# Kernel optimization log

Measured on AMD Instinct MI355X. Metric: run time of the kernel, lower is better.

## Reference

```python
import jax, jax.numpy as jnp
import numpy as np

B, EMB, HID, IN_DIM, STEP = 4096, 256, 256, 128, 128


def setup_inputs() -> dict:
    key = jax.random.key(0)
    ks = jax.random.split(key, 9)
    s1 = 1.0 / np.sqrt(HID)   # torch LSTMCell init: U(-1/sqrt(hidden), 1/sqrt(hidden))
    s2 = 1.0 / np.sqrt(IN_DIM)
    u = lambda k, shape, s: jax.random.uniform(k, shape, jnp.float32, -s, s)
    return {
        "emb_inp": jax.random.normal(ks[0], (B, EMB), jnp.float32),
        # cell1: LSTMCell(EMB -> HID), gate order i,f,g,o
        "W_ih1": u(ks[1], (4 * HID, EMB), s1),
        "W_hh1": u(ks[2], (4 * HID, HID), s1),
        "b_ih1": u(ks[3], (4 * HID,), s1),
        "b_hh1": u(ks[4], (4 * HID,), s1),
        # cell2: LSTMCell(HID -> IN_DIM)
        "W_ih2": u(ks[5], (4 * IN_DIM, HID), s2),
        "W_hh2": u(ks[6], (4 * IN_DIM, IN_DIM), s2),
        "b_ih2": u(ks[7], (4 * IN_DIM,), s2),
        "b_hh2": u(ks[8], (4 * IN_DIM,), s2),
    }


def _lstm_gates(gates, c):
    # torch.nn.LSTMCell gate order: input, forget, cell(g), output
    i, f, g, o = jnp.split(gates, 4, axis=-1)
    c_new = jax.nn.sigmoid(f) * c + jax.nn.sigmoid(i) * jnp.tanh(g)
    h_new = jax.nn.sigmoid(o) * jnp.tanh(c_new)
    return h_new, c_new


def reference(emb_inp, W_ih1, W_hh1, b_ih1, b_hh1, W_ih2, W_hh2, b_ih2, b_hh2):
    batch = emb_inp.shape[0]
    hid = W_hh1.shape[1]
    in_dim = W_hh2.shape[1]
    dt = emb_inp.dtype
    # the same emb_inp is fed at every step -> precompute input-gate preactivations once
    x1 = emb_inp @ W_ih1.T + b_ih1 + b_hh1              # [B, 4*HID]
    b2 = b_ih2 + b_hh2

    init = (jnp.zeros((batch, hid), dt), jnp.zeros((batch, hid), dt),
            jnp.zeros((batch, in_dim), dt), jnp.zeros((batch, in_dim), dt))

    def step_fn(carry, _):
        h0, c0, h1, c1 = carry
        h0, c0 = _lstm_gates(x1 + h0 @ W_hh1.T, c0)
        h1, c1 = _lstm_gates(h0 @ W_ih2.T + b2 + h1 @ W_hh2.T, c1)
        return (h0, c0, h1, c1), h1

    _, ys = jax.lax.scan(step_fn, init, None, length=STEP)  # [STEP, B, IN_DIM]
    return jnp.transpose(ys, (1, 0, 2))                     # [B, STEP, IN_DIM]
```

## Files before the change

kernel.cpp:

```cpp
#include <hip/hip_runtime.h>

typedef __attribute__((ext_vector_type(8))) short bf16x8;
typedef __attribute__((ext_vector_type(4))) short bf16x4;
typedef __attribute__((ext_vector_type(4))) float f32x4;

__device__ __forceinline__ short f2bf(float f) {
  union { float f; unsigned u; } v; v.f = f;
  unsigned r = v.u + 0x7fffu + ((v.u >> 16) & 1u);
  return (short)(r >> 16);
}
__device__ __forceinline__ float sigm(float x) {
  float e = exp2f(-1.44269504f * x);
  return __builtin_amdgcn_rcpf(1.0f + e);
}
__device__ __forceinline__ float tanh_f(float x) {
  float e = exp2f(-2.88539008f * x);
  return __builtin_fmaf(2.0f, __builtin_amdgcn_rcpf(1.0f + e), -1.0f);
}
__device__ __forceinline__ f32x4 splat4(float b){ f32x4 v = {b,b,b,b}; return v; }

__device__ __forceinline__ void ld_b128_sc0(bf16x8* d, const void* p) {
  asm volatile("global_load_dwordx4 %0, %1, off sc0" : "=&v"(*d) : "v"(p));
}
__device__ __forceinline__ void vm_drain_sched() {
  asm volatile("s_waitcnt vmcnt(0)" ::: "memory");
  __builtin_amdgcn_sched_barrier(0);
}

#define R1S   0
#define R2AS  262144
#define R2BS  393216
#define R1IS  458752
#define CTRL_B 1441792
#define H0X_B  1462272
#define H1X_B  5656576

#define H0S 57344
#define H1S 65536
#define OUTS 69632

__global__ __launch_bounds__(256) void pack_w(
    const float* __restrict__ W_ih1, const float* __restrict__ W_hh1,
    const float* __restrict__ W_ih2, const float* __restrict__ W_hh2,
    short* __restrict__ wp) {
  int s = blockIdx.x * 256 + threadIdx.x;
  if (blockIdx.x == 0) {
    unsigned* c = (unsigned*)((char*)wp + CTRL_B);
    #pragma unroll
    for (int k = 0; k < 20; ++k) c[threadIdx.x + k * 256] = 0u;
  }
  if (s >= 90112) return;
  const float* src; int row, K, k0, l;
  if (s < 32768) {
    int mm = s >> 11, r = s & 2047, g = r >> 9, kc = (r >> 6) & 7; l = r & 63;
    row = g*256 + mm*16 + (l & 15); K = 256; k0 = kc*32 + (l>>4)*8; src = W_hh1;
  } else if (s < 49152) {
    int s2 = s - 32768, mm = s2 >> 10, r = s2 & 1023, gh = r >> 9, kc = (r >> 6) & 7; l = r & 63;
    int ul = (l & 15) >> 1, gp = l & 1;
    row = (gh*2+gp)*128 + mm*8 + ul; K = 256; k0 = kc*32 + (l>>4)*8; src = W_ih2;
  } else if (s < 57344) {
    int s3 = s - 49152, mm = s3 >> 9, r = s3 & 511, gh = r >> 8, kc = (r >> 6) & 3; l = r & 63;
    int ul = (l & 15) >> 1, gp = l & 1;
    row = (gh*2+gp)*128 + mm*8 + ul; K = 128; k0 = kc*32 + (l>>4)*8; src = W_hh2;
  } else {
    int s4 = s - 57344, mm = s4 >> 11, r = s4 & 2047, g = r >> 9, kc = (r >> 6) & 7; l = r & 63;
    row = g*256 + mm*16 + (l & 15); K = 256; k0 = kc*32 + (l>>4)*8; src = W_ih1;
  }
  const float* p = src + (size_t)row * K + k0;
  bf16x8 o;
  #pragma unroll
  for (int e = 0; e < 8; ++e) o[e] = f2bf(p[e]);
  *(bf16x8*)(wp + (size_t)s * 8) = o;
}

__global__ __launch_bounds__(512, 2) void lstm_persist(
    const float* __restrict__ emb, const float* __restrict__ b_ih1,
    const float* __restrict__ b_hh1, const float* __restrict__ b_ih2,
    const float* __restrict__ b_hh2, char* __restrict__ ws,
    float* __restrict__ out) {
  extern __shared__ __align__(16) short ldsW[];
  char* ldsB = (char*)ldsW;
  const short* wp = (const short*)ws;
  unsigned* ctrl = (unsigned*)(ws + CTRL_B);
  __shared__ unsigned s_gm;
  const int tid = threadIdx.x, w = tid >> 6, l = tid & 63, l15 = l & 15, l4 = l >> 4;
  const int ul = l15 >> 1, gp = l15 & 1;

  if (tid == 0) {
    unsigned xcc;
    asm volatile("s_getreg_b32 %0, hwreg(HW_REG_XCC_ID)" : "=s"(xcc));
    xcc &= 7u;
    unsigned slot = atomicAdd(&ctrl[xcc * 32], 1u);
    s_gm = ((xcc * 2u + ((slot >> 4) & 1u)) << 8) | (slot & 15u);
  }
  __syncthreads();
  const int group = s_gm >> 8, member = s_gm & 255;

  {
    const char* wpB = (const char*)wp;
    #pragma unroll
    for (int it = 0; it < 7; ++it) {
      int byte = (tid + it * 512) * 16;
      const char* src;
      if (byte < 32768)      src = wpB + (size_t)R1S * 2  + member * 32768 + byte;
      else if (byte < 49152) src = wpB + (size_t)R2AS * 2 + member * 16384 + (byte - 32768);
      else                   src = wpB + (size_t)R2BS * 2 + member * 8192  + (byte - 49152);
      *(f32x4*)(ldsB + byte) = *(const f32x4*)src;
    }
  }
  float b2[2];
  #pragma unroll
  for (int gh = 0; gh < 2; ++gh) {
    int rw = (gh*2+gp)*128 + member*8 + ul;
    b2[gh] = b_ih2[rw] + b_hh2[rw];
  }
  float b1[4];
  #pragma unroll
  for (int g = 0; g < 4; ++g) {
    int rw = g*256 + member*16 + l15;
    b1[g] = b_ih1[rw] + b_hh1[rw];
  }
  __syncthreads();

  const int grow0 = group * 256;
  const int rw0 = w * 32;
  f32x4 x1[2][4];
  #pragma unroll
  for (int m = 0; m < 2; ++m)
    #pragma unroll
    for (int g = 0; g < 4; ++g) x1[m][g] = splat4(b1[g]);
  #pragma unroll
  for (int kc = 0; kc < 8; ++kc) {
    bf16x8 af[2];
    #pragma unroll
    for (int m = 0; m < 2; ++m) {
      const float* ep = emb + (size_t)(grow0 + rw0 + m*16 + l15) * 256 + kc*32 + l4*8;
      f32x4 lo = *(const f32x4*)ep, hi = *(const f32x4*)(ep + 4);
      bf16x8 t8;
      #pragma unroll
      for (int e = 0; e < 4; ++e) { t8[e] = f2bf(lo[e]); t8[e+4] = f2bf(hi[e]); }
      af[m] = t8;
    }
    #pragma unroll
    for (int g = 0; g < 4; ++g) {
      bf16x8 bb = *(const bf16x8*)(wp + R1IS + (((size_t)member*4 + g)*8 + kc)*512 + l*8);
      x1[0][g] = __builtin_amdgcn_mfma_f32_16x16x32_bf16(af[0], bb, x1[0][g], 0, 0, 0);
      x1[1][g] = __builtin_amdgcn_mfma_f32_16x16x32_bf16(af[1], bb, x1[1][g], 0, 0, 0);
    }
  }

  bf16x8 a0[2][8], a1[2][4];
  const bf16x8 ZB = {0,0,0,0,0,0,0,0};
  #pragma unroll
  for (int m = 0; m < 2; ++m) {
    #pragma unroll
    for (int kc = 0; kc < 8; ++kc) a0[m][kc] = ZB;
    #pragma unroll
    for (int kc = 0; kc < 4; ++kc) a1[m][kc] = ZB;
  }
  float c0[2][4] = {};
  float c1[2][2] = {};

  unsigned* flgA = &ctrl[512 + group * 64];
  unsigned* flgB = flgA + 32;
  char* h0x = ws + H0X_B;
  char* h1x = ws + H1X_B;

  #pragma unroll 1
  for (int u = 0; u <= 128; ++u) {
    if (u < 128) {
      vm_drain_sched();
      f32x4 acc1[2][4];
      #pragma unroll
      for (int m = 0; m < 2; ++m)
        #pragma unroll
        for (int g = 0; g < 4; ++g) acc1[m][g] = x1[m][g];
      #pragma unroll
      for (int g = 0; g < 4; ++g)
        #pragma unroll
        for (int kc = 0; kc < 8; ++kc) {
          bf16x8 bb = *(const bf16x8*)(ldsW + (g*8 + kc)*512 + l*8);
          acc1[0][g] = __builtin_amdgcn_mfma_f32_16x16x32_bf16(a0[0][kc], bb, acc1[0][g], 0,0,0);
          acc1[1][g] = __builtin_amdgcn_mfma_f32_16x16x32_bf16(a0[1][kc], bb, acc1[1][g], 0,0,0);
        }
      #pragma unroll
      for (int m = 0; m < 2; ++m)
        #pragma unroll
        for (int r = 0; r < 4; ++r) {
          float iv = acc1[m][0][r], fv = acc1[m][1][r];
          float gv = acc1[m][2][r], ov = acc1[m][3][r];
          float c = sigm(fv) * c0[m][r] + sigm(iv) * tanh_f(gv);
          c0[m][r] = c;
          float h = sigm(ov) * tanh_f(c);
          int row = rw0 + m*16 + l4*4 + r;
          *(short*)(ldsB + H0S + row*32 + l15*2) = f2bf(h);
        }
      {
        char* h0w = h0x + ((size_t)(u & 1) * 16 + group) * 131072;
        int prow = rw0 + (l >> 1);
        int off = prow*32 + (l & 1)*16;
        bf16x8 v = *(const bf16x8*)(ldsB + H0S + off);
        *(bf16x8*)(h0w + member*8192 + off) = v;
      }
      asm volatile("s_waitcnt vmcnt(0)" ::: "memory");
      __syncthreads();
      if (tid == 0)
        __hip_atomic_store(&flgA[member], (unsigned)(u + 1),
                           __ATOMIC_RELAXED, __HIP_MEMORY_SCOPE_AGENT);
    }
    f32x4 acc2[2][2];
    if (u >= 1) {
      if (u >= 2) {
        unsigned tgt = (unsigned)(u - 1); int z = 0;
        while (true) {
          unsigned v = __hip_atomic_load(&flgB[l15], __ATOMIC_RELAXED, __HIP_MEMORY_SCOPE_AGENT);
          if (__all((int)(v >= tgt))) break;
          __builtin_amdgcn_s_sleep(1);
          if (++z > (1 << 20)) break;
        }
        __builtin_amdgcn_sched_barrier(0);
        const char* h1r = h1x + ((size_t)((u - 2) & 1) * 16 + group) * 65536;
        #pragma unroll
        for (int m = 0; m < 2; ++m)
          #pragma unroll
          for (int kc = 0; kc < 4; ++kc)
            ld_b128_sc0(&a1[m][kc], h1r + (kc*4 + l4)*4096 + (rw0 + m*16 + l15)*16);
        vm_drain_sched();
      }
      #pragma unroll
      for (int m = 0; m < 2; ++m)
        #pragma unroll
        for (int gh = 0; gh < 2; ++gh) acc2[m][gh] = splat4(b2[gh]);
      #pragma unroll
      for (int gh = 0; gh < 2; ++gh)
        #pragma unroll
        for (int kc = 0; kc < 8; ++kc) {
          bf16x8 bb = *(const bf16x8*)(ldsW + 16384 + (gh*8 + kc)*512 + l*8);
          acc2[0][gh] = __builtin_amdgcn_mfma_f32_16x16x32_bf16(a0[0][kc], bb, acc2[0][gh], 0,0,0);
          acc2[1][gh] = __builtin_amdgcn_mfma_f32_16x16x32_bf16(a0[1][kc], bb, acc2[1][gh], 0,0,0);
        }
      #pragma unroll
      for (int gh = 0; gh < 2; ++gh)
        #pragma unroll
        for (int kc = 0; kc < 4; ++kc) {
          bf16x8 bb = *(const bf16x8*)(ldsW + 24576 + (gh*4 + kc)*512 + l*8);
          acc2[0][gh] = __builtin_amdgcn_mfma_f32_16x16x32_bf16(a1[0][kc], bb, acc2[0][gh], 0,0,0);
          acc2[1][gh] = __builtin_amdgcn_mfma_f32_16x16x32_bf16(a1[1][kc], bb, acc2[1][gh], 0,0,0);
        }
    }
    if (u < 128) {
      unsigned tgt = (unsigned)(u + 1); int z = 0;
      while (true) {
        unsigned v = __hip_atomic_load(&flgA[l15], __ATOMIC_RELAXED, __HIP_MEMORY_SCOPE_AGENT);
        if (__all((int)(v >= tgt))) break;
        __builtin_amdgcn_s_sleep(1);
        if (++z > (1 << 20)) break;
      }
      __builtin_amdgcn_sched_barrier(0);
      const char* h0r = h0x + ((size_t)(u & 1) * 16 + group) * 131072;
      #pragma unroll
      for (int m = 0; m < 2; ++m)
        #pragma unroll
        for (int kc = 0; kc < 8; ++kc)
          ld_b128_sc0(&a0[m][kc],
                      h0r + (kc*2 + (l4 >> 1))*8192 + (rw0 + m*16 + l15)*32 + (l4 & 1)*16);
      __builtin_amdgcn_sched_barrier(0);
    }
    if (u >= 1) {
      const int t = u - 1;
      #pragma unroll
      for (int m = 0; m < 2; ++m) {
        f32x4 v0 = acc2[m][0], v1 = acc2[m][1];
        #pragma unroll
        for (int rr = 0; rr < 2; ++rr) {
          float s0 = gp ? v0[rr] : v0[2+rr];
          float s1 = gp ? v1[rr] : v1[2+rr];
          float p0 = __shfl_xor(s0, 1, 64);
          float p1 = __shfl_xor(s1, 1, 64);
          float o0 = gp ? v0[2+rr] : v0[rr];
          float o1 = gp ? v1[2+rr] : v1[rr];
          float iv = gp ? p0 : o0, fv = gp ? o0 : p0;
          float gv = gp ? p1 : o1, ov = gp ? o1 : p1;
          float c = sigm(fv) * c1[m][rr] + sigm(iv) * tanh_f(gv);
          c1[m][rr] = c;
          float h = sigm(ov) * tanh_f(c);
          int row = rw0 + m*16 + l4*4 + gp*2 + rr;
          *(short*)(ldsB + H1S + row*16 + ul*2) = f2bf(h);
          *(float*)(ldsB + OUTS + row*32 + ul*4) = h;
        }
      }
      if (u < 128) {
        char* h1w = h1x + ((size_t)(t & 1) * 16 + group) * 65536;
        int prow = rw0 + (l >> 1);
        int off = prow*16 + (l & 1)*8;
        bf16x4 v = *(const bf16x4*)(ldsB + H1S + off);
        *(bf16x4*)(h1w + member*4096 + off) = v;
        asm volatile("s_waitcnt vmcnt(0)" ::: "memory");
        __syncthreads();
        if (tid == 0)
          __hip_atomic_store(&flgB[member], (unsigned)u,
                             __ATOMIC_RELAXED, __HIP_MEMORY_SCOPE_AGENT);
      }
      {
        int prow = rw0 + (l >> 1);
        f32x4 v = *(const f32x4*)(ldsB + OUTS + prow*32 + (l & 1)*16);
        float* op = out + (size_t)(grow0 + prow) * 16384 + t*128 + member*8 + (l & 1)*4;
        __builtin_nontemporal_store(v, (f32x4*)op);
      }
    }
  }
}

extern "C" void kernel_launch(void* const* d_in, const int* in_sizes, int n_in,
                              void* d_out, int out_size, void* d_ws, size_t ws_size,
                              hipStream_t stream) {
  const float* emb   = (const float*)d_in[0];
  const float* W_ih1 = (const float*)d_in[1];
  const float* W_hh1 = (const float*)d_in[2];
  const float* b_ih1 = (const float*)d_in[3];
  const float* b_hh1 = (const float*)d_in[4];
  const float* W_ih2 = (const float*)d_in[5];
  const float* W_hh2 = (const float*)d_in[6];
  const float* b_ih2 = (const float*)d_in[7];
  const float* b_hh2 = (const float*)d_in[8];
  char* ws = (char*)d_ws;
  float* out = (float*)d_out;

  hipFuncSetAttribute((const void*)lstm_persist,
                      hipFuncAttributeMaxDynamicSharedMemorySize, 98304);
  pack_w<<<352, 256, 0, stream>>>(W_ih1, W_hh1, W_ih2, W_hh2, (short*)d_ws);
  lstm_persist<<<256, 512, 98304, stream>>>(emb, b_ih1, b_hh1, b_ih2, b_hh2, ws, out);
}
```

Baseline: 881.6 us.

## Merge two per-step cross-workgroup barriers into one combined flag sync

Replaces the separate flgA/flgB flag handshakes for h0 and h1 with a single per-step flag. Each step now computes cell1 and cell2, publishes both hidden states, and signals once. It then waits once and loads both the next h0 and h1 operands together. This halves the number of global spin-wait barriers on the recurrent critical path, but removes the overlap between the cell2 MMA and the h0 exchange wait.

```diff
diff --git a/kernel.cpp b/kernel.cpp
--- a/kernel.cpp
+++ b/kernel.cpp
@@ -161,15 +161,13 @@
   float c0[2][4] = {};
   float c1[2][2] = {};
 
-  unsigned* flgA = &ctrl[512 + group * 64];
-  unsigned* flgB = flgA + 32;
+  unsigned* flg = &ctrl[512 + group * 64];
   char* h0x = ws + H0X_B;
   char* h1x = ws + H1X_B;
 
   #pragma unroll 1
   for (int u = 0; u <= 128; ++u) {
     if (u < 128) {
-      vm_drain_sched();
       f32x4 acc1[2][4];
       #pragma unroll
       for (int m = 0; m < 2; ++m)
@@ -202,31 +200,10 @@
         bf16x8 v = *(const bf16x8*)(ldsB + H0S + off);
         *(bf16x8*)(h0w + member*8192 + off) = v;
       }
-      asm volatile("s_waitcnt vmcnt(0)" ::: "memory");
-      __syncthreads();
-      if (tid == 0)
-        __hip_atomic_store(&flgA[member], (unsigned)(u + 1),
-                           __ATOMIC_RELAXED, __HIP_MEMORY_SCOPE_AGENT);
-    }
-    f32x4 acc2[2][2];
+    }
     if (u >= 1) {
-      if (u >= 2) {
-        unsigned tgt = (unsigned)(u - 1); int z = 0;
-        while (true) {
-          unsigned v = __hip_atomic_load(&flgB[l15], __ATOMIC_RELAXED, __HIP_MEMORY_SCOPE_AGENT);
-          if (__all((int)(v >= tgt))) break;
-          __builtin_amdgcn_s_sleep(1);
-          if (++z > (1 << 20)) break;
-        }
-        __builtin_amdgcn_sched_barrier(0);
-        const char* h1r = h1x + ((size_t)((u - 2) & 1) * 16 + group) * 65536;
-        #pragma unroll
-        for (int m = 0; m < 2; ++m)
-          #pragma unroll
-          for (int kc = 0; kc < 4; ++kc)
-            ld_b128_sc0(&a1[m][kc], h1r + (kc*4 + l4)*4096 + (rw0 + m*16 + l15)*16);
-        vm_drain_sched();
-      }
+      const int t = u - 1;
+      f32x4 acc2[2][2];
       #pragma unroll
       for (int m = 0; m < 2; ++m)
         #pragma unroll
@@ -247,27 +224,6 @@
           acc2[0][gh] = __builtin_amdgcn_mfma_f32_16x16x32_bf16(a1[0][kc], bb, acc2[0][gh], 0,0,0);
           acc2[1][gh] = __builtin_amdgcn_mfma_f32_16x16x32_bf16(a1[1][kc], bb, acc2[1][gh], 0,0,0);
         }
-    }
-    if (u < 128) {
-      unsigned tgt = (unsigned)(u + 1); int z = 0;
-      while (true) {
-        unsigned v = __hip_atomic_load(&flgA[l15], __ATOMIC_RELAXED, __HIP_MEMORY_SCOPE_AGENT);
-        if (__all((int)(v >= tgt))) break;
-        __builtin_amdgcn_s_sleep(1);
-        if (++z > (1 << 20)) break;
-      }
-      __builtin_amdgcn_sched_barrier(0);
-      const char* h0r = h0x + ((size_t)(u & 1) * 16 + group) * 131072;
-      #pragma unroll
-      for (int m = 0; m < 2; ++m)
-        #pragma unroll
-        for (int kc = 0; kc < 8; ++kc)
-          ld_b128_sc0(&a0[m][kc],
-                      h0r + (kc*2 + (l4 >> 1))*8192 + (rw0 + m*16 + l15)*32 + (l4 & 1)*16);
-      __builtin_amdgcn_sched_barrier(0);
-    }
-    if (u >= 1) {
-      const int t = u - 1;
       #pragma unroll
       for (int m = 0; m < 2; ++m) {
         f32x4 v0 = acc2[m][0], v1 = acc2[m][1];
@@ -295,18 +251,53 @@
         int off = prow*16 + (l & 1)*8;
         bf16x4 v = *(const bf16x4*)(ldsB + H1S + off);
         *(bf16x4*)(h1w + member*4096 + off) = v;
-        asm volatile("s_waitcnt vmcnt(0)" ::: "memory");
-        __syncthreads();
-        if (tid == 0)
-          __hip_atomic_store(&flgB[member], (unsigned)u,
-                             __ATOMIC_RELAXED, __HIP_MEMORY_SCOPE_AGENT);
-      }
-      {
+      }
+    }
+    if (u < 128) {
+      asm volatile("s_waitcnt vmcnt(0)" ::: "memory");
+      __syncthreads();
+      if (tid == 0)
+        __hip_atomic_store(&flg[member], (unsigned)(u + 1),
+                           __ATOMIC_RELAXED, __HIP_MEMORY_SCOPE_AGENT);
+      if (u >= 1) {
+        const int t = u - 1;
         int prow = rw0 + (l >> 1);
         f32x4 v = *(const f32x4*)(ldsB + OUTS + prow*32 + (l & 1)*16);
-        float* op = out + (size_t)(grow0 + prow) * 16384 + t*128 + member*8 + (l & 1)*4;
+        float* op = out + (size_t)(grow0 + prow) * 16384 + (size_t)t*128 + member*8 + (l & 1)*4;
         __builtin_nontemporal_store(v, (f32x4*)op);
       }
+      {
+        unsigned tgt = (unsigned)(u + 1); int z = 0;
+        while (true) {
+          unsigned v = __hip_atomic_load(&flg[l15], __ATOMIC_RELAXED, __HIP_MEMORY_SCOPE_AGENT);
+          if (__all((int)(v >= tgt))) break;
+          __builtin_amdgcn_s_sleep(1);
+          if (++z > (1 << 20)) break;
+        }
+      }
+      __builtin_amdgcn_sched_barrier(0);
+      const char* h0r = h0x + ((size_t)(u & 1) * 16 + group) * 131072;
+      #pragma unroll
+      for (int m = 0; m < 2; ++m)
+        #pragma unroll
+        for (int kc = 0; kc < 8; ++kc)
+          ld_b128_sc0(&a0[m][kc],
+                      h0r + (kc*2 + (l4 >> 1))*8192 + (rw0 + m*16 + l15)*32 + (l4 & 1)*16);
+      if (u >= 1) {
+        const char* h1r = h1x + ((size_t)((u - 1) & 1) * 16 + group) * 65536;
+        #pragma unroll
+        for (int m = 0; m < 2; ++m)
+          #pragma unroll
+          for (int kc = 0; kc < 4; ++kc)
+            ld_b128_sc0(&a1[m][kc], h1r + (kc*4 + l4)*4096 + (rw0 + m*16 + l15)*16);
+      }
+      vm_drain_sched();
+    } else {
+      const int t = 127;
+      int prow = rw0 + (l >> 1);
+      f32x4 v = *(const f32x4*)(ldsB + OUTS + prow*32 + (l & 1)*16);
+      float* op = out + (size_t)(grow0 + prow) * 16384 + (size_t)t*128 + member*8 + (l & 1)*4;
+      __builtin_nontemporal_store(v, (f32x4*)op);
     }
   }
 }
```

Result: slower. 1.388 ms (+57.4%).
